# Kernel optimization log

Measured on AMD Instinct MI355X. Metric: run time of the kernel, lower is better.

Reference implementation:

```python
import jax, jax.numpy as jnp
import numpy as np

N_NODES = 100000
N_EDGES = 1600000
N_GRAPHS = 256
NODE_DIM = 64
EDGE_DIM = 64
HIDDEN = 128
VOCAB = 128
N_CONV = 3
R_MIN, R_MAX = 1.0, 6.0
LN_EPS = 1e-5


def layer_norm(x, g, b):
    mu = jnp.mean(x, axis=-1, keepdims=True)
    var = jnp.mean(jnp.square(x - mu), axis=-1, keepdims=True)
    return (x - mu) * jax.lax.rsqrt(var + LN_EPS) * g + b


def setup_inputs() -> dict:
    key = jax.random.key(0)
    ks = jax.random.split(key, 16)
    inp = {}
    inp["numbers"] = jax.random.randint(ks[0], (N_NODES,), 0, VOCAB)
    inp["edge_index"] = jax.random.randint(ks[1], (2, N_EDGES), 0, N_NODES)
    inp["edge_length"] = jax.random.uniform(ks[2], (N_EDGES,), minval=R_MIN, maxval=R_MAX, dtype=jnp.float32)
    inp["batch"] = jnp.sort(jax.random.randint(ks[3], (N_NODES,), 0, N_GRAPHS))
    s = 0.1
    inp["embed_table"] = jax.random.normal(ks[4], (VOCAB, NODE_DIM), jnp.float32)
    inp["Wf"] = jax.random.normal(ks[5], (N_CONV, 2 * NODE_DIM + EDGE_DIM, NODE_DIM), jnp.float32) * s
    inp["bf"] = jnp.zeros((N_CONV, NODE_DIM), jnp.float32)
    inp["Ws"] = jax.random.normal(ks[6], (N_CONV, 2 * NODE_DIM + EDGE_DIM, NODE_DIM), jnp.float32) * s
    inp["bs"] = jnp.zeros((N_CONV, NODE_DIM), jnp.float32)
    inp["ln_g"] = jnp.ones((N_CONV, NODE_DIM), jnp.float32)
    inp["ln_b"] = jnp.zeros((N_CONV, NODE_DIM), jnp.float32)
    inp["olp_W1"] = jax.random.normal(ks[7], (NODE_DIM, HIDDEN), jnp.float32) * s
    inp["olp_b1"] = jnp.zeros((HIDDEN,), jnp.float32)
    inp["olp_g1"] = jnp.ones((HIDDEN,), jnp.float32)
    inp["olp_bt1"] = jnp.zeros((HIDDEN,), jnp.float32)
    inp["olp_W2"] = jax.random.normal(ks[8], (HIDDEN, HIDDEN), jnp.float32) * s
    inp["olp_b2"] = jnp.zeros((HIDDEN,), jnp.float32)
    inp["olp_g2"] = jnp.ones((HIDDEN,), jnp.float32)
    inp["olp_bt2"] = jnp.zeros((HIDDEN,), jnp.float32)
    inp["W_out"] = jax.random.normal(ks[9], (HIDDEN, 1), jnp.float32) * s
    inp["b_out"] = jnp.zeros((1,), jnp.float32)
    return inp


def reference(numbers, edge_index, edge_length, batch, embed_table,
              Wf, bf, Ws, bs, ln_g, ln_b,
              olp_W1, olp_b1, olp_g1, olp_bt1,
              olp_W2, olp_b2, olp_g2, olp_bt2,
              W_out, b_out):
    n_nodes = numbers.shape[0]
    # Gaussian edge expansion: exp(-0.5*((d - centers)/step)^2)  -> [E, edge_dim]
    centers = jnp.linspace(R_MIN, R_MAX, EDGE_DIM, dtype=jnp.float32)
    step = (R_MAX - R_MIN) / EDGE_DIM
    edge_attrs = jnp.exp(-0.5 * jnp.square((edge_length[:, None] - centers) / step))

    x = embed_table[numbers]                      # [N, node_dim]
    src, tgt = edge_index[0], edge_index[1]

    for i in range(N_CONV):
        z = jnp.concatenate([x[src], x[tgt], edge_attrs], axis=-1)  # [E, 2d+e]
        gate = jax.nn.sigmoid(z @ Wf[i] + bf[i]) * jax.nn.softplus(z @ Ws[i] + bs[i])
        msg = jax.ops.segment_sum(gate, src, num_segments=n_nodes)  # reduce='add'
        x = x + layer_norm(msg, ln_g[i], ln_b[i])

    # hidden OLPs: Linear -> LayerNorm -> Softplus (dropout identity at eval)
    h = jax.nn.softplus(layer_norm(x @ olp_W1 + olp_b1, olp_g1, olp_bt1))
    h = jax.nn.softplus(layer_norm(h @ olp_W2 + olp_b2, olp_g2, olp_bt2))
    e = h @ W_out + b_out                          # [N, 1]

    # per_atom_target=True -> segment mean over graphs
    sums = jax.ops.segment_sum(e, batch, num_segments=N_GRAPHS)      # [G, 1]
    cnt = jax.ops.segment_sum(jnp.ones((n_nodes,), e.dtype), batch, num_segments=N_GRAPHS)
    energy = sums / jnp.maximum(cnt, 1.0)[:, None]
    return energy
```

## Files before the change

### kernel.cpp

```cpp
#include <hip/hip_runtime.h>
#include <hip/hip_fp16.h>
#include <math.h>

#define NNODES 100000
#define NEDGES 1600000
#define NGRAPH 256
#define NCONV  3
#define TBL    4096
#define CHUNK  512
#define NCHUNK 196
#define CAP    9216
#define R_MIN_ 1.0f
#define R_MAX_ 6.0f
#define LOG2E  1.4426950408889634f

typedef _Float16 f16x8 __attribute__((ext_vector_type(8)));
typedef float f32x4 __attribute__((ext_vector_type(4)));
union HF { float4 f4; f16x8 h8; __half2 q[4]; };

__device__ __forceinline__ float softplus_f(float x){
  return fmaxf(x, 0.f) + __logf(1.f + __expf(-fabsf(x)));
}

__global__ void k_embed(const int* __restrict__ numbers, const float* __restrict__ embed,
                        float* __restrict__ x){
  int i = blockIdx.x*256 + threadIdx.x;
  if (i >= NNODES*64) return;
  int n = i >> 6, c = i & 63;
  x[i] = embed[numbers[n]*64 + c];
}

__global__ void k_prep(const float* __restrict__ W1, const float* __restrict__ W2,
                       __half* __restrict__ Wm1, __half* __restrict__ Wm2,
                       float2* __restrict__ lutg, int* __restrict__ ccur,
                       float* __restrict__ gsum, int* __restrict__ gcnt){
  int b = blockIdx.x, t = threadIdx.x;
  if (b == 64){
    __shared__ float cv[513];
    for (int i = t; i < 513; i += 256){
      float z = -16.f + (float)i * (1.f/16.f);
      cv[i] = log2f(1.f + exp2f(z));
    }
    __syncthreads();
    for (int i = t; i < 512; i += 256)
      lutg[i] = make_float2(cv[i], cv[i+1]-cv[i]);
    if (t < NCHUNK) ccur[t] = t * CAP;
    if (t < NGRAPH){ gsum[t] = 0.f; gcnt[t] = 0; }
    return;
  }
  int i = b*256 + t;
  if (i < 8192){
    int ct = i >> 10;
    int kt = (i >> 9) & 1;
    int lane = (i >> 3) & 63;
    int e = i & 7;
    int k = kt*32 + (lane>>4)*8 + e;
    int c = ct*16 + (lane&15);
    Wm1[i] = __float2half_rn(W1[k*128 + c]);
  }
  {
    int ct = i >> 11;
    int kt = (i >> 9) & 3;
    int lane = (i >> 3) & 63;
    int e = i & 7;
    int k = kt*32 + (lane>>4)*8 + e;
    int c = ct*16 + (lane&15);
    Wm2[i] = __float2half_rn(W2[k*128 + c]);
  }
}

__global__ void k_bin(const int* __restrict__ src, const int* __restrict__ tgt,
                      const float* __restrict__ elen, int* ccur,
                      int2* __restrict__ eb){
  __shared__ int lcnt[NCHUNK];
  __shared__ int lbase[NCHUNK];
  __shared__ int loff[NCHUNK];
  int t = threadIdx.x;
  int e0 = blockIdx.x * 2048;
  if (t < NCHUNK){ lcnt[t] = 0; loff[t] = 0; }
  __syncthreads();
  #pragma unroll
  for (int k = 0; k < 8; k++){
    int e = e0 + k*256 + t;
    if (e < NEDGES) atomicAdd(&lcnt[src[e] / CHUNK], 1);
  }
  __syncthreads();
  if (t < NCHUNK && lcnt[t] > 0) lbase[t] = atomicAdd(&ccur[t], lcnt[t]);
  __syncthreads();
  #pragma unroll
  for (int k = 0; k < 8; k++){
    int e = e0 + k*256 + t;
    if (e < NEDGES){
      int s = src[e];
      int c = s / CHUNK;
      int r = atomicAdd(&loff[c], 1);
      float key = (elen[e] - R_MIN_) * ((float)(TBL-1)/(R_MAX_-R_MIN_));
      key = fmaxf(key, 0.f);
      int idx = (int)(key + 0.5f);
      if (idx > TBL-1) idx = TBL-1;
      eb[lbase[c] + r] = make_int2(((s & (CHUNK-1)) << 17) | tgt[e], idx);
    }
  }
}

__global__ void k_fine(const int* __restrict__ ccur, const int2* __restrict__ eb,
                       int2* __restrict__ ep, int* __restrict__ offs,
                       int* __restrict__ deg){
  __shared__ int lcnt[CHUNK];
  __shared__ int lsc[CHUNK];
  int c = blockIdx.x;
  int t = threadIdx.x;
  int n0 = c * CHUNK;
  int n1 = min(n0 + CHUNK, NNODES);
  int cnt = n1 - n0;
  int j0 = c * CAP;
  int j1 = ccur[c];
  lcnt[t] = 0;
  __syncthreads();
  for (int e = j0 + t; e < j1; e += 512)
    atomicAdd(&lcnt[((unsigned)eb[e].x) >> 17], 1);
  __syncthreads();
  lsc[t] = lcnt[t];
  __syncthreads();
  for (int d = 1; d < 512; d <<= 1){
    int v = (t >= d) ? lsc[t-d] : 0;
    __syncthreads();
    lsc[t] += v;
    __syncthreads();
  }
  int excl = lsc[t] - lcnt[t];
  if (t < cnt){ offs[n0 + t] = j0 + excl; deg[n0 + t] = lcnt[t]; }
  __syncthreads();
  lcnt[t] = j0 + excl;
  __syncthreads();
  for (int e = j0 + t; e < j1; e += 512){
    int2 rec = eb[e];
    int sl = ((unsigned)rec.x) >> 17;
    int pos = atomicAdd(&lcnt[sl], 1);
    ep[pos] = make_int2(rec.x & 0x1FFFF, rec.y);
  }
}

__global__ void k_gauss(const float* __restrict__ Wf, const float* __restrict__ bf,
                        const float* __restrict__ Ws, const float* __restrict__ bs,
                        __half* __restrict__ Gth){
  __shared__ float attr[64];
  int bi = blockIdx.x;
  int i = bi / TBL, r = bi % TBL;
  int t = threadIdx.x;
  float d = R_MIN_ + (R_MAX_-R_MIN_) * (float)r / (float)(TBL-1);
  if (t < 64){
    float cj = 1.f + 5.f * (float)t / 63.f;
    float u = (d - cj) * (64.f/5.f);
    attr[t] = __expf(-0.5f*u*u);
  }
  __syncthreads();
  int c = t >> 1;
  int side = t & 1;
  const float* W = (side ? Ws : Wf) + i*192*64 + 128*64 + c;
  float acc = (side ? bs : bf)[i*64 + c];
  #pragma unroll 8
  for (int j = 0; j < 64; j++) acc = fmaf(attr[j], W[j*64], acc);
  Gth[((size_t)i*TBL + r)*128 + t] = __float2half_rn(acc * LOG2E);
}

__global__ void k_wcat(const float* __restrict__ Wf, const float* __restrict__ Ws,
                       __half* __restrict__ WmC){
  int idx = blockIdx.x*256 + threadIdx.x;
  if (idx >= 3*16384) return;
  int i = idx / 16384;
  int rem = idx & 16383;
  int ct = rem >> 10;
  int kt = (rem >> 9) & 1;
  int lane = (rem >> 3) & 63;
  int e = rem & 7;
  int col = ct*16 + (lane & 15);
  int part = col >> 6;
  int ch = col & 63;
  int k = kt*32 + (lane >> 4)*8 + e;
  int row = ((part >> 1) ? 64 : 0) + k;
  const float* W = ((part & 1) ? Ws : Wf) + i*192*64;
  WmC[idx] = __float2half_rn(W[row*64 + ch]);
}

__global__ void k_ntrans(const float* __restrict__ x, const __half* __restrict__ WmC,
                         __half2* __restrict__ pqh){
  __shared__ __half xh[32*72];
  int n0 = blockIdx.x * 32;
  int t = threadIdx.x;
  int w = t >> 6, lane = t & 63;
  int lg = lane >> 4, lc = lane & 15;
  {
    int n = t >> 3, g = t & 7;
    const float4* xp = (const float4*)(x + (size_t)(n0 + n)*64 + g*8);
    float4 a = xp[0], b = xp[1];
    HF hh;
    hh.q[0] = __float22half2_rn(make_float2(a.x, a.y));
    hh.q[1] = __float22half2_rn(make_float2(a.z, a.w));
    hh.q[2] = __float22half2_rn(make_float2(b.x, b.y));
    hh.q[3] = __float22half2_rn(make_float2(b.z, b.w));
    *(float4*)(xh + n*72 + g*8) = hh.f4;
  }
  __syncthreads();
  HF a[2][2];
  #pragma unroll
  for (int m = 0; m < 2; m++)
    #pragma unroll
    for (int kt = 0; kt < 2; kt++)
      a[m][kt].f4 = *(const float4*)(xh + (m*16 + lc)*72 + kt*32 + lg*8);
  const float4* wb = (const float4*)WmC;
  f32x4 acc[4][2];
  #pragma unroll
  for (int p4 = 0; p4 < 4; p4++){
    int ct = p4*4 + w;
    HF b0, b1;
    b0.f4 = wb[(ct*2 + 0)*64 + lane];
    b1.f4 = wb[(ct*2 + 1)*64 + lane];
    #pragma unroll
    for (int m = 0; m < 2; m++){
      f32x4 c = {0.f, 0.f, 0.f, 0.f};
      c = __builtin_amdgcn_mfma_f32_16x16x32_f16(a[m][0].h8, b0.h8, c, 0, 0, 0);
      c = __builtin_amdgcn_mfma_f32_16x16x32_f16(a[m][1].h8, b1.h8, c, 0, 0, 0);
      acc[p4][m] = c;
    }
  }
  #pragma unroll
  for (int m = 0; m < 2; m++)
    #pragma unroll
    for (int r = 0; r < 4; r++){
      int node = n0 + m*16 + lg*4 + r;
      int ch = w*16 + lc;
      __half2 hp = __floats2half2_rn(acc[0][m][r]*LOG2E, acc[1][m][r]*LOG2E);
      __half2 hq = __floats2half2_rn(acc[2][m][r]*LOG2E, acc[3][m][r]*LOG2E);
      pqh[(size_t)node*128 + ch]      = hp;
      pqh[(size_t)node*128 + 64 + ch] = hq;
    }
}

__global__ void k_edge(const __half2* __restrict__ pqh,
                       const int* __restrict__ offs, const int* __restrict__ deg,
                       const int2* __restrict__ ep,
                       const __half* __restrict__ Gth, const float* __restrict__ lng,
                       const float* __restrict__ lnb, const float2* __restrict__ lutg,
                       float* __restrict__ x){
  __shared__ float2 lut[512];
  {
    ((float4*)lut)[threadIdx.x] = ((const float4*)lutg)[threadIdx.x];
  }
  __syncthreads();
  int wid  = (blockIdx.x*256 + threadIdx.x) >> 6;
  int lane = threadIdx.x & 63;
  int n = wid;
  int j0 = __builtin_amdgcn_readfirstlane(offs[n]);
  int j1 = j0 + __builtin_amdgcn_readfirstlane(deg[n]);
  int nfull = (j1 - j0) >> 3;
  int2 eb8[8];
  if (nfull > 0){
    #pragma unroll
    for (int i = 0; i < 8; i++) eb8[i] = ep[j0 + i];
  }
  float2 pp = __half22float2(pqh[(size_t)n*128 + lane]);
  float pf = pp.x, ps = pp.y;
  float pso = fmaf(ps, 16.f, 256.f);
  const char* pqb = (const char*)pqh;
  const char* gtb = (const char*)Gth;
  unsigned qob = 256u + ((unsigned)lane << 2);
  unsigned lob = (unsigned)lane << 2;
  float acc = 0.f;
  int u = j0;
  for (int b = 0; b < nfull; b++){
    __half2 qr[8], gr[8];
    #pragma unroll
    for (int i = 0; i < 8; i++){
      qr[i] = *(const __half2*)(pqb + ((((unsigned)eb8[i].x) << 9) + qob));
      gr[i] = *(const __half2*)(gtb + ((((unsigned)eb8[i].y) << 8) + lob));
    }
    if (b + 1 < nfull){
      #pragma unroll
      for (int i = 0; i < 8; i++) eb8[i] = ep[u + 8 + i];
    }
    #pragma unroll
    for (int i = 0; i < 8; i++){
      float2 z = __half22float2(__hadd2(qr[i], gr[i]));
      float sig = __builtin_amdgcn_rcpf(1.f + __builtin_amdgcn_exp2f(-(pf + z.x)));
      float xj = __builtin_amdgcn_fmed3f(fmaf(z.y, 16.f, pso), 0.f, 511.36f);
      int i2 = (int)xj;
      float f2 = __builtin_amdgcn_fractf(xj);
      float2 e2 = lut[i2];
      float zs = ps + z.y;
      float sp = fmaxf(zs, fmaf(e2.y, f2, e2.x));
      acc = fmaf(sig, sp, acc);
    }
    u += 8;
  }
  for (; u < j1; u++){
    int2 e = ep[u];
    __half2 q = *(const __half2*)(pqb + ((((unsigned)e.x) << 9) + qob));
    __half2 g = *(const __half2*)(gtb + ((((unsigned)e.y) << 8) + lob));
    float2 z = __half22float2(__hadd2(q, g));
    float sig = __builtin_amdgcn_rcpf(1.f + __builtin_amdgcn_exp2f(-(pf + z.x)));
    float xj = __builtin_amdgcn_fmed3f(fmaf(z.y, 16.f, pso), 0.f, 511.36f);
    int i2 = (int)xj;
    float f2 = __builtin_amdgcn_fractf(xj);
    float2 e2 = lut[i2];
    float zs = ps + z.y;
    float sp = fmaxf(zs, fmaf(e2.y, f2, e2.x));
    acc = fmaf(sig, sp, acc);
  }
  float s1 = acc, s2 = acc*acc;
  #pragma unroll
  for (int o = 32; o > 0; o >>= 1){ s1 += __shfl_xor(s1, o, 64); s2 += __shfl_xor(s2, o, 64); }
  float mu  = s1 * (1.f/64.f);
  float var = s2 * (1.f/64.f) - mu*mu;
  float inv = rsqrtf(fmaxf(var, 0.f) + 1e-5f);
  float y = (acc - mu) * inv * lng[lane] + lnb[lane];
  x[(size_t)n*64 + lane] += y;
}

__global__ void k_head(const float* __restrict__ x,
                       const __half* __restrict__ Wm1, const float* __restrict__ b1,
                       const float* __restrict__ g1, const float* __restrict__ bt1,
                       const __half* __restrict__ Wm2, const float* __restrict__ b2,
                       const float* __restrict__ g2, const float* __restrict__ bt2,
                       const float* __restrict__ Wout, const int* __restrict__ batch,
                       float* gsum, int* gcnt){
  __shared__ __half xh[32*72];
  __shared__ __half hs[32*136];
  __shared__ float red[4][32][2];
  __shared__ float stat[32][2];
  __shared__ float es[32];
  int n0 = blockIdx.x * 32;
  int t = threadIdx.x;
  int w = t >> 6, lane = t & 63;
  int lg = lane >> 4, lc = lane & 15;
  int col0 = w*32 + lc, col1 = w*32 + 16 + lc;

  {
    int n = t >> 3, g = t & 7;
    const float4* xp = (const float4*)(x + (size_t)(n0 + n)*64 + g*8);
    float4 a = xp[0], b = xp[1];
    HF hh;
    hh.q[0] = __float22half2_rn(make_float2(a.x, a.y));
    hh.q[1] = __float22half2_rn(make_float2(a.z, a.w));
    hh.q[2] = __float22half2_rn(make_float2(b.x, b.y));
    hh.q[3] = __float22half2_rn(make_float2(b.z, b.w));
    *(float4*)(xh + n*72 + g*8) = hh.f4;
  }
  __syncthreads();

  f32x4 acc[2][2];
  {
    HF a[2][2], b[2][2];
    #pragma unroll
    for (int m = 0; m < 2; m++)
      #pragma unroll
      for (int kt = 0; kt < 2; kt++)
        a[m][kt].f4 = *(const float4*)(xh + (m*16 + lc)*72 + kt*32 + lg*8);
    const float4* wb = (const float4*)Wm1;
    #pragma unroll
    for (int ct = 0; ct < 2; ct++)
      #pragma unroll
      for (int kt = 0; kt < 2; kt++)
        b[ct][kt].f4 = wb[(((w*2 + ct)*2 + kt)*64) + lane];
    #pragma unroll
    for (int m = 0; m < 2; m++)
      #pragma unroll
      for (int ct = 0; ct < 2; ct++){
        f32x4 c = {0.f, 0.f, 0.f, 0.f};
        c = __builtin_amdgcn_mfma_f32_16x16x32_f16(a[m][0].h8, b[ct][0].h8, c, 0, 0, 0);
        c = __builtin_amdgcn_mfma_f32_16x16x32_f16(a[m][1].h8, b[ct][1].h8, c, 0, 0, 0);
        acc[m][ct] = c;
      }
  }
  {
    float bv0 = b1[col0], bv1 = b1[col1];
    #pragma unroll
    for (int m = 0; m < 2; m++)
      #pragma unroll
      for (int r = 0; r < 4; r++){
        acc[m][0][r] += bv0; acc[m][1][r] += bv1;
        float a0 = acc[m][0][r], a1 = acc[m][1][r];
        float s1 = a0 + a1, s2 = a0*a0 + a1*a1;
        #pragma unroll
        for (int o = 1; o < 16; o <<= 1){ s1 += __shfl_xor(s1, o, 64); s2 += __shfl_xor(s2, o, 64); }
        if (lc == 0){ int row = m*16 + lg*4 + r; red[w][row][0] = s1; red[w][row][1] = s2; }
      }
  }
  __syncthreads();
  if (t < 32){
    float s1 = red[0][t][0] + red[1][t][0] + red[2][t][0] + red[3][t][0];
    float s2 = red[0][t][1] + red[1][t][1] + red[2][t][1] + red[3][t][1];
    float mu = s1 * (1.f/128.f);
    float var = s2 * (1.f/128.f) - mu*mu;
    stat[t][0] = mu;
    stat[t][1] = rsqrtf(fmaxf(var, 0.f) + 1e-5f);
  }
  __syncthreads();
  {
    float g1a = g1[col0], g1b = g1[col1], b1a = bt1[col0], b1b = bt1[col1];
    #pragma unroll
    for (int m = 0; m < 2; m++)
      #pragma unroll
      for (int r = 0; r < 4; r++){
        int row = m*16 + lg*4 + r;
        float mu = stat[row][0], inv = stat[row][1];
        float y0 = (acc[m][0][r] - mu)*inv*g1a + b1a;
        float y1 = (acc[m][1][r] - mu)*inv*g1b + b1b;
        hs[row*136 + col0] = __float2half_rn(softplus_f(y0));
        hs[row*136 + col1] = __float2half_rn(softplus_f(y1));
      }
  }
  __syncthreads();

  f32x4 acc2[2][2];
  {
    HF b[2][4];
    const float4* wb = (const float4*)Wm2;
    #pragma unroll
    for (int ct = 0; ct < 2; ct++)
      #pragma unroll
      for (int kt = 0; kt < 4; kt++)
        b[ct][kt].f4 = wb[(((w*2 + ct)*4 + kt)*64) + lane];
    #pragma unroll
    for (int m = 0; m < 2; m++){
      f32x4 c0 = {0.f,0.f,0.f,0.f}, c1 = {0.f,0.f,0.f,0.f};
      #pragma unroll
      for (int kt = 0; kt < 4; kt++){
        HF av; av.f4 = *(const float4*)(hs + (m*16 + lc)*136 + kt*32 + lg*8);
        c0 = __builtin_amdgcn_mfma_f32_16x16x32_f16(av.h8, b[0][kt].h8, c0, 0, 0, 0);
        c1 = __builtin_amdgcn_mfma_f32_16x16x32_f16(av.h8, b[1][kt].h8, c1, 0, 0, 0);
      }
      acc2[m][0] = c0; acc2[m][1] = c1;
    }
  }
  {
    float bv0 = b2[col0], bv1 = b2[col1];
    #pragma unroll
    for (int m = 0; m < 2; m++)
      #pragma unroll
      for (int r = 0; r < 4; r++){
        acc2[m][0][r] += bv0; acc2[m][1][r] += bv1;
        float a0 = acc2[m][0][r], a1 = acc2[m][1][r];
        float s1 = a0 + a1, s2 = a0*a0 + a1*a1;
        #pragma unroll
        for (int o = 1; o < 16; o <<= 1){ s1 += __shfl_xor(s1, o, 64); s2 += __shfl_xor(s2, o, 64); }
        if (lc == 0){ int row = m*16 + lg*4 + r; red[w][row][0] = s1; red[w][row][1] = s2; }
      }
  }
  __syncthreads();
  if (t < 32){
    float s1 = red[0][t][0] + red[1][t][0] + red[2][t][0] + red[3][t][0];
    float s2 = red[0][t][1] + red[1][t][1] + red[2][t][1] + red[3][t][1];
    float mu = s1 * (1.f/128.f);
    float var = s2 * (1.f/128.f) - mu*mu;
    stat[t][0] = mu;
    stat[t][1] = rsqrtf(fmaxf(var, 0.f) + 1e-5f);
  }
  __syncthreads();
  {
    float g2a = g2[col0], g2b = g2[col1], b2a = bt2[col0], b2b = bt2[col1];
    float woa = Wout[col0], wob = Wout[col1];
    #pragma unroll
    for (int m = 0; m < 2; m++)
      #pragma unroll
      for (int r = 0; r < 4; r++){
        int row = m*16 + lg*4 + r;
        float mu = stat[row][0], inv = stat[row][1];
        float e = softplus_f((acc2[m][0][r] - mu)*inv*g2a + b2a) * woa
                + softplus_f((acc2[m][1][r] - mu)*inv*g2b + b2b) * wob;
        #pragma unroll
        for (int o = 1; o < 16; o <<= 1) e += __shfl_xor(e, o, 64);
        if (lc == 0) red[w][row][0] = e;
      }
  }
  __syncthreads();
  if (t < 32) es[t] = red[0][t][0] + red[1][t][0] + red[2][t][0] + red[3][t][0];
  __syncthreads();

  if (t < 32){
    int node = n0 + t;
    int g = batch[node];
    bool head = (t == 0) || (batch[node-1] != g);
    if (head){
      float s = 0.f; int c = 0;
      int j = t;
      while (j < 32 && batch[n0+j] == g){ s += es[j]; c++; j++; }
      atomicAdd(&gsum[g], s);
      atomicAdd(&gcnt[g], c);
    }
  }
}

__global__ void k_final(const float* __restrict__ gsum, const int* __restrict__ gcnt,
                        const float* __restrict__ bout, float* __restrict__ out){
  int g = threadIdx.x;
  if (g < NGRAPH)
    out[g] = gsum[g] / fmaxf((float)gcnt[g], 1.f) + bout[0];
}

extern "C" void kernel_launch(void* const* d_in, const int* in_sizes, int n_in,
                              void* d_out, int out_size, void* d_ws, size_t ws_size,
                              hipStream_t stream){
  const int*   numbers = (const int*)d_in[0];
  const int*   eidx    = (const int*)d_in[1];
  const float* elen    = (const float*)d_in[2];
  const int*   batch   = (const int*)d_in[3];
  const float* embed   = (const float*)d_in[4];
  const float* Wf      = (const float*)d_in[5];
  const float* bf      = (const float*)d_in[6];
  const float* Ws      = (const float*)d_in[7];
  const float* bs      = (const float*)d_in[8];
  const float* lng     = (const float*)d_in[9];
  const float* lnb     = (const float*)d_in[10];
  const float* W1      = (const float*)d_in[11];
  const float* b1      = (const float*)d_in[12];
  const float* g1      = (const float*)d_in[13];
  const float* bt1     = (const float*)d_in[14];
  const float* W2      = (const float*)d_in[15];
  const float* b2      = (const float*)d_in[16];
  const float* g2      = (const float*)d_in[17];
  const float* bt2     = (const float*)d_in[18];
  const float* Wout    = (const float*)d_in[19];
  const float* bout    = (const float*)d_in[20];
  const int* src = eidx;
  const int* tgt = eidx + NEDGES;

  float*   x    = (float*)d_ws;
  __half2* pqh  = (__half2*)(x + (size_t)NNODES*64);
  __half*  Gth  = (__half*)(pqh + (size_t)NNODES*128);
  __half*  WmC  = Gth + (size_t)3*TBL*128;
  __half*  Wm1  = WmC + (size_t)3*16384;
  __half*  Wm2  = Wm1 + 8192;
  float2*  lutg = (float2*)(Wm2 + 16384);
  int2*    ep   = (int2*)(lutg + 1024);
  int2*    ebuf = ep + (size_t)NCHUNK*CAP;
  int*     offs = (int*)(ebuf + (size_t)NCHUNK*CAP);
  int*     deg  = offs + NNODES;
  int*     ccur = deg + NNODES;
  float*   gsum = (float*)(ccur + 256);
  int*     gcnt = (int*)(gsum + NGRAPH);
  float*   out  = (float*)d_out;

  k_prep  <<<65, 256, 0, stream>>>(W1, W2, Wm1, Wm2, lutg, ccur, gsum, gcnt);
  k_embed <<<(NNODES*64+255)/256, 256, 0, stream>>>(numbers, embed, x);

  k_bin   <<<(NEDGES+2047)/2048, 256, 0, stream>>>(src, tgt, elen, ccur, ebuf);
  k_fine  <<<NCHUNK, 512, 0, stream>>>(ccur, ebuf, ep, offs, deg);

  k_gauss <<<3*TBL, 128, 0, stream>>>(Wf, bf, Ws, bs, Gth);
  k_wcat  <<<(3*16384+255)/256, 256, 0, stream>>>(Wf, Ws, WmC);

  for (int i = 0; i < NCONV; i++){
    k_ntrans<<<NNODES/32, 256, 0, stream>>>(x, WmC + (size_t)i*16384, pqh);
    k_edge  <<<NNODES/4, 256, 0, stream>>>(pqh, offs, deg, ep,
                                           Gth + (size_t)i*TBL*128,
                                           lng + i*64, lnb + i*64, lutg, x);
  }

  k_head<<<NNODES/32, 256, 0, stream>>>(x, Wm1, b1, g1, bt1,
                                        Wm2, b2, g2, bt2, Wout, batch, gsum, gcnt);
  k_final<<<1, 256, 0, stream>>>(gsum, gcnt, bout, out);
}
```

Before: 541.6 us.

## Merge embed and weight-cat kernels into prep; pad edge tail into masked batch

Folds the embedding gather and the weight concatenation/fp16 packing into the k_prep launch, removing two kernel launches. In k_edge, the scalar remainder loop for the last deg%8 edges is replaced by one more 8-wide batch that clamps edge indices to the last valid edge and zero-masks the extra contributions. This keeps the tail loads batched and pipelined, at the cost of redundant gathers and math for padded lanes.

```diff
diff --git a/kernel.cpp b/kernel.cpp
--- a/kernel.cpp
+++ b/kernel.cpp
@@ -22,19 +22,40 @@
   return fmaxf(x, 0.f) + __logf(1.f + __expf(-fabsf(x)));
 }
 
-__global__ void k_embed(const int* __restrict__ numbers, const float* __restrict__ embed,
-                        float* __restrict__ x){
-  int i = blockIdx.x*256 + threadIdx.x;
-  if (i >= NNODES*64) return;
-  int n = i >> 6, c = i & 63;
-  x[i] = embed[numbers[n]*64 + c];
-}
-
-__global__ void k_prep(const float* __restrict__ W1, const float* __restrict__ W2,
+__global__ void k_prep(const int* __restrict__ numbers, const float* __restrict__ embed,
+                       float* __restrict__ x,
+                       const float* __restrict__ Wf, const float* __restrict__ Ws,
+                       __half* __restrict__ WmC,
+                       const float* __restrict__ W1, const float* __restrict__ W2,
                        __half* __restrict__ Wm1, __half* __restrict__ Wm2,
                        float2* __restrict__ lutg, int* __restrict__ ccur,
                        float* __restrict__ gsum, int* __restrict__ gcnt){
   int b = blockIdx.x, t = threadIdx.x;
+  if (b >= 257){
+    int i = (b - 257)*256 + t;
+    if (i < NNODES*64){
+      int n = i >> 6, c = i & 63;
+      x[i] = embed[numbers[n]*64 + c];
+    }
+    return;
+  }
+  if (b >= 65){
+    int idx = (b - 65)*256 + t;
+    int i = idx / 16384;
+    int rem = idx & 16383;
+    int ct = rem >> 10;
+    int kt = (rem >> 9) & 1;
+    int lane = (rem >> 3) & 63;
+    int e = rem & 7;
+    int col = ct*16 + (lane & 15);
+    int part = col >> 6;
+    int ch = col & 63;
+    int k = kt*32 + (lane >> 4)*8 + e;
+    int row = ((part >> 1) ? 64 : 0) + k;
+    const float* W = ((part & 1) ? Ws : Wf) + i*192*64;
+    WmC[idx] = __float2half_rn(W[row*64 + ch]);
+    return;
+  }
   if (b == 64){
     __shared__ float cv[513];
     for (int i = t; i < 513; i += 256){
@@ -164,25 +185,6 @@
   Gth[((size_t)i*TBL + r)*128 + t] = __float2half_rn(acc * LOG2E);
 }
 
-__global__ void k_wcat(const float* __restrict__ Wf, const float* __restrict__ Ws,
-                       __half* __restrict__ WmC){
-  int idx = blockIdx.x*256 + threadIdx.x;
-  if (idx >= 3*16384) return;
-  int i = idx / 16384;
-  int rem = idx & 16383;
-  int ct = rem >> 10;
-  int kt = (rem >> 9) & 1;
-  int lane = (rem >> 3) & 63;
-  int e = rem & 7;
-  int col = ct*16 + (lane & 15);
-  int part = col >> 6;
-  int ch = col & 63;
-  int k = kt*32 + (lane >> 4)*8 + e;
-  int row = ((part >> 1) ? 64 : 0) + k;
-  const float* W = ((part & 1) ? Ws : Wf) + i*192*64;
-  WmC[idx] = __float2half_rn(W[row*64 + ch]);
-}
-
 __global__ void k_ntrans(const float* __restrict__ x, const __half* __restrict__ WmC,
                          __half2* __restrict__ pqh){
   __shared__ __half xh[32*72];
@@ -252,12 +254,14 @@
   int lane = threadIdx.x & 63;
   int n = wid;
   int j0 = __builtin_amdgcn_readfirstlane(offs[n]);
-  int j1 = j0 + __builtin_amdgcn_readfirstlane(deg[n]);
-  int nfull = (j1 - j0) >> 3;
+  int dg = __builtin_amdgcn_readfirstlane(deg[n]);
+  int j1 = j0 + dg;
+  int nb = (dg + 7) >> 3;
+  int jl = j1 - 1;
   int2 eb8[8];
-  if (nfull > 0){
-    #pragma unroll
-    for (int i = 0; i < 8; i++) eb8[i] = ep[j0 + i];
+  if (nb > 0){
+    #pragma unroll
+    for (int i = 0; i < 8; i++) eb8[i] = ep[min(j0 + i, jl)];
   }
   float2 pp = __half22float2(pqh[(size_t)n*128 + lane]);
   float pf = pp.x, ps = pp.y;
@@ -267,45 +271,47 @@
   unsigned qob = 256u + ((unsigned)lane << 2);
   unsigned lob = (unsigned)lane << 2;
   float acc = 0.f;
-  int u = j0;
-  for (int b = 0; b < nfull; b++){
+  for (int b = 0; b < nb; b++){
+    int base = j0 + b*8;
     __half2 qr[8], gr[8];
     #pragma unroll
     for (int i = 0; i < 8; i++){
       qr[i] = *(const __half2*)(pqb + ((((unsigned)eb8[i].x) << 9) + qob));
       gr[i] = *(const __half2*)(gtb + ((((unsigned)eb8[i].y) << 8) + lob));
     }
-    if (b + 1 < nfull){
-      #pragma unroll
-      for (int i = 0; i < 8; i++) eb8[i] = ep[u + 8 + i];
-    }
-    #pragma unroll
-    for (int i = 0; i < 8; i++){
-      float2 z = __half22float2(__hadd2(qr[i], gr[i]));
-      float sig = __builtin_amdgcn_rcpf(1.f + __builtin_amdgcn_exp2f(-(pf + z.x)));
-      float xj = __builtin_amdgcn_fmed3f(fmaf(z.y, 16.f, pso), 0.f, 511.36f);
-      int i2 = (int)xj;
-      float f2 = __builtin_amdgcn_fractf(xj);
-      float2 e2 = lut[i2];
-      float zs = ps + z.y;
-      float sp = fmaxf(zs, fmaf(e2.y, f2, e2.x));
-      acc = fmaf(sig, sp, acc);
-    }
-    u += 8;
-  }
-  for (; u < j1; u++){
-    int2 e = ep[u];
-    __half2 q = *(const __half2*)(pqb + ((((unsigned)e.x) << 9) + qob));
-    __half2 g = *(const __half2*)(gtb + ((((unsigned)e.y) << 8) + lob));
-    float2 z = __half22float2(__hadd2(q, g));
-    float sig = __builtin_amdgcn_rcpf(1.f + __builtin_amdgcn_exp2f(-(pf + z.x)));
-    float xj = __builtin_amdgcn_fmed3f(fmaf(z.y, 16.f, pso), 0.f, 511.36f);
-    int i2 = (int)xj;
-    float f2 = __builtin_amdgcn_fractf(xj);
-    float2 e2 = lut[i2];
-    float zs = ps + z.y;
-    float sp = fmaxf(zs, fmaf(e2.y, f2, e2.x));
-    acc = fmaf(sig, sp, acc);
+    if (b + 1 < nb){
+      #pragma unroll
+      for (int i = 0; i < 8; i++) eb8[i] = ep[min(base + 8 + i, jl)];
+    }
+    if (base + 8 <= j1){
+      #pragma unroll
+      for (int i = 0; i < 8; i++){
+        float2 z = __half22float2(__hadd2(qr[i], gr[i]));
+        float sig = __builtin_amdgcn_rcpf(1.f + __builtin_amdgcn_exp2f(-(pf + z.x)));
+        float xj = __builtin_amdgcn_fmed3f(fmaf(z.y, 16.f, pso), 0.f, 511.36f);
+        int i2 = (int)xj;
+        float f2 = __builtin_amdgcn_fractf(xj);
+        float2 e2 = lut[i2];
+        float zs = ps + z.y;
+        float sp = fmaxf(zs, fmaf(e2.y, f2, e2.x));
+        acc = fmaf(sig, sp, acc);
+      }
+    } else {
+      int rem = j1 - base;
+      #pragma unroll
+      for (int i = 0; i < 8; i++){
+        float m = (i < rem) ? 1.f : 0.f;
+        float2 z = __half22float2(__hadd2(qr[i], gr[i]));
+        float sig = __builtin_amdgcn_rcpf(1.f + __builtin_amdgcn_exp2f(-(pf + z.x)));
+        float xj = __builtin_amdgcn_fmed3f(fmaf(z.y, 16.f, pso), 0.f, 511.36f);
+        int i2 = (int)xj;
+        float f2 = __builtin_amdgcn_fractf(xj);
+        float2 e2 = lut[i2];
+        float zs = ps + z.y;
+        float sp = fmaxf(zs, fmaf(e2.y, f2, e2.x));
+        acc = fmaf(sig * m, sp, acc);
+      }
+    }
   }
   float s1 = acc, s2 = acc*acc;
   #pragma unroll
@@ -541,14 +547,14 @@
   int*     gcnt = (int*)(gsum + NGRAPH);
   float*   out  = (float*)d_out;
 
-  k_prep  <<<65, 256, 0, stream>>>(W1, W2, Wm1, Wm2, lutg, ccur, gsum, gcnt);
-  k_embed <<<(NNODES*64+255)/256, 256, 0, stream>>>(numbers, embed, x);
+  k_prep  <<<257 + (NNODES*64+255)/256, 256, 0, stream>>>(
+            numbers, embed, x, Wf, Ws, WmC, W1, W2, Wm1, Wm2,
+            lutg, ccur, gsum, gcnt);
 
   k_bin   <<<(NEDGES+2047)/2048, 256, 0, stream>>>(src, tgt, elen, ccur, ebuf);
   k_fine  <<<NCHUNK, 512, 0, stream>>>(ccur, ebuf, ep, offs, deg);
 
   k_gauss <<<3*TBL, 128, 0, stream>>>(Wf, bf, Ws, bs, Gth);
-  k_wcat  <<<(3*16384+255)/256, 256, 0, stream>>>(Wf, Ws, WmC);
 
   for (int i = 0; i < NCONV; i++){
     k_ntrans<<<NNODES/32, 256, 0, stream>>>(x, WmC + (size_t)i*16384, pqh);
```

Result: no change. 549.2 us (+1.4%).
